# Optimization experiments

Measured on AMD Instinct MI355X. Metric: run time of the kernel, lower is better.

## Reference

```python
import jax, jax.numpy as jnp
import numpy as np

EPS = 1e-8  # torch F.cosine_similarity eps


def _normalize(x):
    # x: [N, D]; clamp norm at eps like torch cosine_similarity
    n = jnp.linalg.norm(x, axis=-1, keepdims=True)
    return x / jnp.maximum(n, EPS)


def setup_inputs() -> dict:
    key = jax.random.key(0)
    k1, k2 = jax.random.split(key)
    N, D = 8192, 256
    return {
        "model_output": jax.random.normal(k1, (N, D), dtype=jnp.float32),
        "targets": jax.random.normal(k2, (N, D), dtype=jnp.float32),
        "weight": 1.0,
    }


def reference(model_output, targets, weight):
    # Pairwise cosine similarity via normalize + matmul (same math as
    # broadcasted cosine_similarity, without the O(N^2*D) intermediate).
    o = _normalize(model_output)          # [N, D]
    t = _normalize(targets)               # [N, D]
    sim_o = o @ o.T                       # [N, N]
    sim_t = t @ t.T                       # [N, N]
    n = sim_o.shape[0]
    mask = jnp.eye(n, dtype=bool)
    sim_o = jnp.where(mask, 0.0, sim_o)
    sim_t = jnp.where(mask, 0.0, sim_t)
    loss = jnp.mean((sim_o - sim_t) ** 2)
    return weight * loss
```

## Files before the change

### kernel.cpp

```cpp
#include <hip/hip_runtime.h>
#include <hip/hip_bf16.h>
#include <math.h>


#define N_ROWS 8192
#define DDIM   256
#define NC     16
#define KC     (N_ROWS / NC)
#define KS     64
#define ITERS  (KC / KS)
#define TW     64
#define PART_STRIDE (3 * 16 * 4096)

#define INV_O_OFF 16
#define INV_T_OFF (16 + N_ROWS)
#define PART_FOFF (16 + 2 * N_ROWS)

typedef __bf16 bf16x8 __attribute__((ext_vector_type(8)));
typedef short  short8 __attribute__((ext_vector_type(8)));
typedef float  f32x16 __attribute__((ext_vector_type(16)));

__device__ inline unsigned short f2bu(float x) {
    __hip_bfloat16 h = __float2bfloat16(x);
    return __builtin_bit_cast(unsigned short, h);
}
__device__ inline float u2f(unsigned short u) {
    unsigned int v = ((unsigned int)u) << 16;
    return __builtin_bit_cast(float, v);
}

__global__ void norms_kernel(const float* __restrict__ O,
                             const float* __restrict__ T,
                             float* __restrict__ ws) {
    if (blockIdx.x == 0 && threadIdx.x == 0) ws[0] = 0.0f;
    int wave = (blockIdx.x * blockDim.x + threadIdx.x) >> 6;
    int lane = threadIdx.x & 63;
    const float* src;
    float* dst;
    int row;
    if (wave < N_ROWS) { src = O; row = wave;          dst = ws + INV_O_OFF; }
    else               { src = T; row = wave - N_ROWS; dst = ws + INV_T_OFF; }
    float4 v = *reinterpret_cast<const float4*>(src + (size_t)row * DDIM + lane * 4);
    float ss = v.x * v.x + v.y * v.y + v.z * v.z + v.w * v.w;
    #pragma unroll
    for (int off = 32; off > 0; off >>= 1) ss += __shfl_down(ss, off);
    if (lane == 0) dst[row] = 1.0f / fmaxf(sqrtf(ss), 1e-8f);
}

__global__ __launch_bounds__(256) void gram_kernel(const float* __restrict__ O,
                                                   const float* __restrict__ T,
                                                   float* __restrict__ ws) {
    const float* inv_o = ws + INV_O_OFF;
    const float* inv_t = ws + INV_T_OFF;
    unsigned short* part = (unsigned short*)(ws + PART_FOFF);

    int bid = blockIdx.x;
    int ti = bid & 15, c = bid >> 4;
    int tm = ti >> 2, tn = ti & 3;
    int tid = threadIdx.x;
    int lane = tid & 63, wid = tid >> 6;
    int wm = wid >> 1, wn = wid & 1;
    int k0 = c * KC;

    __shared__ unsigned short lds[2][4][KS * TW];

    float4 rv[4][4];
    float  iv[4][2];

    f32x16 acc_oo, acc_tt, acc_ot;
    #pragma unroll
    for (int e = 0; e < 16; ++e) { acc_oo[e] = 0.f; acc_tt[e] = 0.f; acc_ot[e] = 0.f; }

    auto stage_load = [&](int it) {
        int kb = k0 + it * KS;
        #pragma unroll
        for (int q = 0; q < 4; ++q) {
            int u = tid + q * 256;
            int k = u >> 4;
            int f0 = (u & 15) * 4;
            int row = kb + k;
            iv[q][0] = inv_o[row];
            iv[q][1] = inv_t[row];
            #pragma unroll
            for (int s = 0; s < 4; ++s) {
                const float* M = (s >> 1) ? T : O;
                int ft = (s & 1) ? tn : tm;
                rv[q][s] = *reinterpret_cast<const float4*>(
                    M + (size_t)row * DDIM + ft * TW + f0);
            }
        }
    };
    auto stage_write = [&](int buf) {
        #pragma unroll
        for (int q = 0; q < 4; ++q) {
            int u = tid + q * 256;
            int k = u >> 4;
            int f0 = (u & 15) * 4;
            int fx = f0 ^ (((k >> 3) & 1) << 5);
            #pragma unroll
            for (int s = 0; s < 4; ++s) {
                float sc = iv[q][s >> 1];
                float4 v = rv[q][s];
                ushort4 w;
                w.x = f2bu(v.x * sc); w.y = f2bu(v.y * sc);
                w.z = f2bu(v.z * sc); w.w = f2bu(v.w * sc);
                *reinterpret_cast<ushort4*>(&lds[buf][s][k * TW + fx]) = w;
            }
        }
    };
    auto ldfrag = [&](const unsigned short* sl, int kb, int fx) -> bf16x8 {
        short8 t;
        #pragma unroll
        for (int j = 0; j < 8; ++j) t[j] = (short)sl[(kb + j) * TW + fx];
        return __builtin_bit_cast(bf16x8, t);
    };

    stage_load(0);
    stage_write(0);
    __syncthreads();

    for (int it = 0; it < ITERS; ++it) {
        int cur = it & 1;
        if (it + 1 < ITERS) stage_load(it + 1);
        #pragma unroll
        for (int kk = 0; kk < 4; ++kk) {
            int kb = kk * 16 + ((lane >> 5) << 3);
            int sw = ((kb >> 3) & 1) << 5;
            int fmx = ((wm << 5) + (lane & 31)) ^ sw;
            int fnx = ((wn << 5) + (lane & 31)) ^ sw;
            bf16x8 ao = ldfrag(&lds[cur][0][0], kb, fmx);
            bf16x8 bo = ldfrag(&lds[cur][1][0], kb, fnx);
            bf16x8 at = ldfrag(&lds[cur][2][0], kb, fmx);
            bf16x8 bt = ldfrag(&lds[cur][3][0], kb, fnx);
            acc_oo = __builtin_amdgcn_mfma_f32_32x32x16_bf16(ao, bo, acc_oo, 0, 0, 0);
            acc_tt = __builtin_amdgcn_mfma_f32_32x32x16_bf16(at, bt, acc_tt, 0, 0, 0);
            acc_ot = __builtin_amdgcn_mfma_f32_32x32x16_bf16(ao, bt, acc_ot, 0, 0, 0);
        }
        if (it + 1 < ITERS) stage_write(cur ^ 1);
        __syncthreads();
    }

    unsigned int tb = (unsigned int)(c * 16 + ti) * 3;
    #pragma unroll
    for (int reg = 0; reg < 16; ++reg) {
        int row = (reg & 3) + 8 * (reg >> 2) + ((lane >> 5) << 2);
        int col = lane & 31;
        int idx = (wm * 32 + row) * TW + (wn * 32 + col);
        part[(size_t)(tb + 0) * 4096 + idx] = f2bu(acc_oo[reg]);
        part[(size_t)(tb + 1) * 4096 + idx] = f2bu(acc_tt[reg]);
        part[(size_t)(tb + 2) * 4096 + idx] = f2bu(acc_ot[reg]);
    }
}

__global__ void reduce_kernel(float* __restrict__ ws) {
    const unsigned short* part = (const unsigned short*)(ws + PART_FOFF);
    int gid = blockIdx.x * blockDim.x + threadIdx.x;
    int base = gid * 4;
    float s0 = 0.f, s1 = 0.f, s2 = 0.f, s3 = 0.f;
    for (int cc = 0; cc < NC; ++cc) {
        ushort4 u = *reinterpret_cast<const ushort4*>(&part[(size_t)cc * PART_STRIDE + base]);
        s0 += u2f(u.x); s1 += u2f(u.y); s2 += u2f(u.z); s3 += u2f(u.w);
    }
    int g = (base >> 12) % 3;
    float s = s0 * s0 + s1 * s1 + s2 * s2 + s3 * s3;
    if (g == 2) s = -2.0f * s;
    #pragma unroll
    for (int off = 32; off > 0; off >>= 1) s += __shfl_down(s, off);
    __shared__ float wsum[4];
    int lane = threadIdx.x & 63, w = threadIdx.x >> 6;
    if (lane == 0) wsum[w] = s;
    __syncthreads();
    if (threadIdx.x == 0)
        atomicAdd(&ws[0], wsum[0] + wsum[1] + wsum[2] + wsum[3]);
}

__global__ void finalize_kernel(const float* __restrict__ ws,
                                const float* __restrict__ weight,
                                float* __restrict__ out) {
    out[0] = ws[0] * weight[0] / ((float)N_ROWS * (float)N_ROWS);
}

extern "C" void kernel_launch(void* const* d_in, const int* in_sizes, int n_in,
                              void* d_out, int out_size, void* d_ws, size_t ws_size,
                              hipStream_t stream) {
    const float* O = (const float*)d_in[0];
    const float* T = (const float*)d_in[1];
    const float* W = (const float*)d_in[2];
    float* out = (float*)d_out;
    float* ws = (float*)d_ws;

    norms_kernel<<<(2 * N_ROWS) / 4, 256, 0, stream>>>(O, T, ws);
    gram_kernel<<<16 * NC, 256, 0, stream>>>(O, T, ws);
    reduce_kernel<<<(PART_STRIDE / 4) / 256, 256, 0, stream>>>(ws);
    finalize_kernel<<<1, 1, 0, stream>>>(ws, W, out);
}
```

Measured before the change: 33.17 us.

## Pre-normalize and transpose inputs to bf16, stage via direct global-to-LDS loads

```diff
diff --git a/kernel.cpp b/kernel.cpp
--- a/kernel.cpp
+++ b/kernel.cpp
@@ -5,20 +5,20 @@
 
 #define N_ROWS 8192
 #define DDIM   256
-#define NC     16
+#define NC     32
 #define KC     (N_ROWS / NC)
 #define KS     64
-#define ITERS  (KC / KS)
-#define TW     64
-#define PART_STRIDE (3 * 16 * 4096)
+#define NITER  (KC / KS)
+#define PART_STRIDE 196608
 
-#define INV_O_OFF 16
-#define INV_T_OFF (16 + N_ROWS)
-#define PART_FOFF (16 + 2 * N_ROWS)
+#define OBT_UOFF  32
+#define MAT_USZ   (DDIM * N_ROWS)
+#define PART_UOFF (OBT_UOFF + 2 * MAT_USZ)
 
 typedef __bf16 bf16x8 __attribute__((ext_vector_type(8)));
 typedef short  short8 __attribute__((ext_vector_type(8)));
 typedef float  f32x16 __attribute__((ext_vector_type(16)));
+typedef unsigned int u32;
 
 __device__ inline unsigned short f2bu(float x) {
     __hip_bfloat16 h = __float2bfloat16(x);
@@ -28,116 +28,106 @@
     unsigned int v = ((unsigned int)u) << 16;
     return __builtin_bit_cast(float, v);
 }
-
-__global__ void norms_kernel(const float* __restrict__ O,
-                             const float* __restrict__ T,
-                             float* __restrict__ ws) {
-    if (blockIdx.x == 0 && threadIdx.x == 0) ws[0] = 0.0f;
-    int wave = (blockIdx.x * blockDim.x + threadIdx.x) >> 6;
-    int lane = threadIdx.x & 63;
-    const float* src;
-    float* dst;
-    int row;
-    if (wave < N_ROWS) { src = O; row = wave;          dst = ws + INV_O_OFF; }
-    else               { src = T; row = wave - N_ROWS; dst = ws + INV_T_OFF; }
-    float4 v = *reinterpret_cast<const float4*>(src + (size_t)row * DDIM + lane * 4);
-    float ss = v.x * v.x + v.y * v.y + v.z * v.z + v.w * v.w;
-    #pragma unroll
-    for (int off = 32; off > 0; off >>= 1) ss += __shfl_down(ss, off);
-    if (lane == 0) dst[row] = 1.0f / fmaxf(sqrtf(ss), 1e-8f);
+__device__ inline void gload_lds16(const void* g, void* l) {
+    __builtin_amdgcn_global_load_lds(
+        (const __attribute__((address_space(1))) u32*)g,
+        (__attribute__((address_space(3))) u32*)l, 16, 0, 0);
 }
 
-__global__ __launch_bounds__(256) void gram_kernel(const float* __restrict__ O,
-                                                   const float* __restrict__ T,
-                                                   float* __restrict__ ws) {
-    const float* inv_o = ws + INV_O_OFF;
-    const float* inv_t = ws + INV_T_OFF;
-    unsigned short* part = (unsigned short*)(ws + PART_FOFF);
+__global__ __launch_bounds__(256) void transpose_kernel(const float* __restrict__ O,
+                                                        const float* __restrict__ T,
+                                                        float* __restrict__ ws) {
+    if (blockIdx.x == 0 && threadIdx.x == 0) ws[0] = 0.0f;
+    int b = blockIdx.x;
+    const float* src = (b & 1) ? T : O;
+    unsigned short* dst = (unsigned short*)ws + OBT_UOFF + (size_t)(b & 1) * MAT_USZ;
+    int kb = (b >> 1) * 32;
+    __shared__ unsigned short lt[32][260];
+    int w = threadIdx.x >> 6, l = threadIdx.x & 63;
+    #pragma unroll
+    for (int j = 0; j < 8; ++j) {
+        int r = j * 4 + w;
+        float4 v = *reinterpret_cast<const float4*>(src + (size_t)(kb + r) * DDIM + l * 4);
+        float ss = v.x * v.x + v.y * v.y + v.z * v.z + v.w * v.w;
+        #pragma unroll
+        for (int off = 32; off > 0; off >>= 1) ss += __shfl_xor(ss, off);
+        float inv = 1.0f / fmaxf(sqrtf(ss), 1e-8f);
+        ushort4 u;
+        u.x = f2bu(v.x * inv); u.y = f2bu(v.y * inv);
+        u.z = f2bu(v.z * inv); u.w = f2bu(v.w * inv);
+        *reinterpret_cast<ushort4*>(&lt[r][l * 4]) = u;
+    }
+    __syncthreads();
+    int f = threadIdx.x;
+    #pragma unroll
+    for (int s = 0; s < 8; ++s) {
+        ushort4 u;
+        u.x = lt[s * 4 + 0][f]; u.y = lt[s * 4 + 1][f];
+        u.z = lt[s * 4 + 2][f]; u.w = lt[s * 4 + 3][f];
+        *reinterpret_cast<ushort4*>(&dst[(size_t)f * N_ROWS + kb + s * 4]) = u;
+    }
+}
+
+__global__ __launch_bounds__(256) void gram_kernel(float* __restrict__ ws) {
+    const unsigned short* obt = (const unsigned short*)ws + OBT_UOFF;
+    unsigned short* part = (unsigned short*)ws + PART_UOFF;
 
     int bid = blockIdx.x;
     int ti = bid & 15, c = bid >> 4;
     int tm = ti >> 2, tn = ti & 3;
-    int tid = threadIdx.x;
-    int lane = tid & 63, wid = tid >> 6;
+    int tid = threadIdx.x, lane = tid & 63, wid = tid >> 6;
     int wm = wid >> 1, wn = wid & 1;
     int k0 = c * KC;
 
-    __shared__ unsigned short lds[2][4][KS * TW];
-
-    float4 rv[4][4];
-    float  iv[4][2];
+    __shared__ __align__(16) unsigned short lds[2][4][KS * 64];
 
     f32x16 acc_oo, acc_tt, acc_ot;
     #pragma unroll
     for (int e = 0; e < 16; ++e) { acc_oo[e] = 0.f; acc_tt[e] = 0.f; acc_ot[e] = 0.f; }
 
-    auto stage_load = [&](int it) {
+    int sl = wid;
+    int mat = sl >> 1;
+    int ft = (sl & 1) ? tn : tm;
+    const unsigned short* slab_src =
+        obt + (size_t)mat * MAT_USZ + (size_t)(ft * 64) * N_ROWS;
+    int frow = lane >> 3;
+    int swz8 = ((lane & 7) ^ (frow & 7)) * 8;
+
+    auto stage = [&](int buf, int it) {
         int kb = k0 + it * KS;
+        const unsigned short* base = slab_src + kb + (size_t)frow * N_ROWS + swz8;
+        unsigned short* ld = &lds[buf][sl][0];
         #pragma unroll
-        for (int q = 0; q < 4; ++q) {
-            int u = tid + q * 256;
-            int k = u >> 4;
-            int f0 = (u & 15) * 4;
-            int row = kb + k;
-            iv[q][0] = inv_o[row];
-            iv[q][1] = inv_t[row];
-            #pragma unroll
-            for (int s = 0; s < 4; ++s) {
-                const float* M = (s >> 1) ? T : O;
-                int ft = (s & 1) ? tn : tm;
-                rv[q][s] = *reinterpret_cast<const float4*>(
-                    M + (size_t)row * DDIM + ft * TW + f0);
-            }
-        }
-    };
-    auto stage_write = [&](int buf) {
-        #pragma unroll
-        for (int q = 0; q < 4; ++q) {
-            int u = tid + q * 256;
-            int k = u >> 4;
-            int f0 = (u & 15) * 4;
-            int fx = f0 ^ (((k >> 3) & 1) << 5);
-            #pragma unroll
-            for (int s = 0; s < 4; ++s) {
-                float sc = iv[q][s >> 1];
-                float4 v = rv[q][s];
-                ushort4 w;
-                w.x = f2bu(v.x * sc); w.y = f2bu(v.y * sc);
-                w.z = f2bu(v.z * sc); w.w = f2bu(v.w * sc);
-                *reinterpret_cast<ushort4*>(&lds[buf][s][k * TW + fx]) = w;
-            }
-        }
-    };
-    auto ldfrag = [&](const unsigned short* sl, int kb, int fx) -> bf16x8 {
-        short8 t;
-        #pragma unroll
-        for (int j = 0; j < 8; ++j) t[j] = (short)sl[(kb + j) * TW + fx];
-        return __builtin_bit_cast(bf16x8, t);
+        for (int i = 0; i < 8; ++i)
+            gload_lds16(base + (size_t)(i * 8) * N_ROWS, ld + i * 512);
     };
 
-    stage_load(0);
-    stage_write(0);
+    int fm = wm * 32 + (lane & 31);
+    int fn = wn * 32 + (lane & 31);
+    int jhalf = lane >> 5;
+    auto frag = [&](int buf, int s, int fl, int kk) -> bf16x8 {
+        int j0 = kk * 2 + jhalf;
+        const unsigned short* p = &lds[buf][s][fl * 64 + ((j0 ^ (fl & 7)) * 8)];
+        return __builtin_bit_cast(bf16x8, *reinterpret_cast<const short8*>(p));
+    };
+
+    stage(0, 0);
     __syncthreads();
-
-    for (int it = 0; it < ITERS; ++it) {
-        int cur = it & 1;
-        if (it + 1 < ITERS) stage_load(it + 1);
+    int cur = 0;
+    for (int it = 0; it < NITER; ++it) {
+        if (it + 1 < NITER) stage(cur ^ 1, it + 1);
         #pragma unroll
         for (int kk = 0; kk < 4; ++kk) {
-            int kb = kk * 16 + ((lane >> 5) << 3);
-            int sw = ((kb >> 3) & 1) << 5;
-            int fmx = ((wm << 5) + (lane & 31)) ^ sw;
-            int fnx = ((wn << 5) + (lane & 31)) ^ sw;
-            bf16x8 ao = ldfrag(&lds[cur][0][0], kb, fmx);
-            bf16x8 bo = ldfrag(&lds[cur][1][0], kb, fnx);
-            bf16x8 at = ldfrag(&lds[cur][2][0], kb, fmx);
-            bf16x8 bt = ldfrag(&lds[cur][3][0], kb, fnx);
+            bf16x8 ao = frag(cur, 0, fm, kk);
+            bf16x8 bo = frag(cur, 1, fn, kk);
+            bf16x8 at = frag(cur, 2, fm, kk);
+            bf16x8 bt = frag(cur, 3, fn, kk);
             acc_oo = __builtin_amdgcn_mfma_f32_32x32x16_bf16(ao, bo, acc_oo, 0, 0, 0);
             acc_tt = __builtin_amdgcn_mfma_f32_32x32x16_bf16(at, bt, acc_tt, 0, 0, 0);
             acc_ot = __builtin_amdgcn_mfma_f32_32x32x16_bf16(ao, bt, acc_ot, 0, 0, 0);
         }
-        if (it + 1 < ITERS) stage_write(cur ^ 1);
         __syncthreads();
+        cur ^= 1;
     }
 
     unsigned int tb = (unsigned int)(c * 16 + ti) * 3;
@@ -145,7 +135,7 @@
     for (int reg = 0; reg < 16; ++reg) {
         int row = (reg & 3) + 8 * (reg >> 2) + ((lane >> 5) << 2);
         int col = lane & 31;
-        int idx = (wm * 32 + row) * TW + (wn * 32 + col);
+        int idx = (wm * 32 + row) * 64 + (wn * 32 + col);
         part[(size_t)(tb + 0) * 4096 + idx] = f2bu(acc_oo[reg]);
         part[(size_t)(tb + 1) * 4096 + idx] = f2bu(acc_tt[reg]);
         part[(size_t)(tb + 2) * 4096 + idx] = f2bu(acc_ot[reg]);
@@ -153,7 +143,7 @@
 }
 
 __global__ void reduce_kernel(float* __restrict__ ws) {
-    const unsigned short* part = (const unsigned short*)(ws + PART_FOFF);
+    const unsigned short* part = (const unsigned short*)ws + PART_UOFF;
     int gid = blockIdx.x * blockDim.x + threadIdx.x;
     int base = gid * 4;
     float s0 = 0.f, s1 = 0.f, s2 = 0.f, s3 = 0.f;
@@ -189,8 +179,8 @@
     float* out = (float*)d_out;
     float* ws = (float*)d_ws;
 
-    norms_kernel<<<(2 * N_ROWS) / 4, 256, 0, stream>>>(O, T, ws);
-    gram_kernel<<<16 * NC, 256, 0, stream>>>(O, T, ws);
-    reduce_kernel<<<(PART_STRIDE / 4) / 256, 256, 0, stream>>>(ws);
+    transpose_kernel<<<512, 256, 0, stream>>>(O, T, ws);
+    gram_kernel<<<16 * NC, 256, 0, stream>>>(ws);
+    reduce_kernel<<<192, 256, 0, stream>>>(ws);
     finalize_kernel<<<1, 1, 0, stream>>>(ws, W, out);
 }
```

New measurement: 31.39 us. 1.06x faster.
